# Kernel tuning notes

Hardware: AMD Instinct MI355X
Metric: run time of the kernel (lower is better)

The kernel has to match this reference:

```python
import jax, jax.numpy as jnp
import numpy as np

N = 8192          # number of candidate boxes
NUM_CLASSES = 80  # COCO-style class count
IOU_THRESHOLD = 0.45


def setup_inputs() -> dict:
    key = jax.random.key(0)
    k1, k2, k3, k4 = jax.random.split(key, 4)
    # valid xyxy boxes: top-left in [0,1000), width/height in [1,101)
    xy = jax.random.uniform(k1, (N, 2)) * 1000.0
    wh = jax.random.uniform(k2, (N, 2)) * 100.0 + 1.0
    boxes = jnp.concatenate([xy, xy + wh], axis=1)            # [N,4]
    scores = jax.random.uniform(k3, (N,))                     # [N], all > 0
    idxs = jax.random.randint(k4, (N,), 0, NUM_CLASSES)       # [N] class ids
    return {"boxes": boxes, "scores": scores, "idxs": idxs}


def _nms_keep_mask(boxes, scores, iou_thr):
    """Greedy NMS (torchvision semantics) on a single set of boxes.
    Returns a boolean keep mask in the ORIGINAL box order."""
    n = boxes.shape[0]
    order = jnp.argsort(-scores)          # score-descending priority
    b = boxes[order]                      # [n,4]
    area = (b[:, 2] - b[:, 0]) * (b[:, 3] - b[:, 1])
    lt = jnp.maximum(b[:, None, :2], b[None, :, :2])   # [n,n,2]
    rb = jnp.minimum(b[:, None, 2:], b[None, :, 2:])   # [n,n,2]
    wh = jnp.clip(rb - lt, 0.0)
    inter = wh[..., 0] * wh[..., 1]                    # [n,n]
    iou = inter / (area[:, None] + area[None, :] - inter)
    over = iou > iou_thr                               # [n,n] bool
    lower_priority = jnp.arange(n)

    def body(i, suppressed):
        kept_i = jnp.logical_not(suppressed[i])
        # a kept box suppresses all lower-priority boxes it overlaps too much
        return suppressed | (kept_i & over[i] & (lower_priority > i))

    suppressed = jax.lax.fori_loop(0, n, body, jnp.zeros((n,), bool))
    # scatter keep decisions back to original order
    return jnp.zeros((n,), bool).at[order].set(~suppressed)


def reference(boxes, scores, idxs):
    iou_threshold = IOU_THRESHOLD
    # per-class coordinate offsets make boxes of different classes disjoint,
    # so one global NMS == the per-class NMS loop of the torch module
    max_coordinate = boxes.max()
    offsets = idxs.astype(boxes.dtype) * (max_coordinate + 1.0)
    boxes_for_nms = boxes + offsets[:, None]
    keep_mask = _nms_keep_mask(boxes_for_nms, scores, iou_threshold)
    # suppressed boxes get score 0 (all real scores are > 0), so after the
    # descending sort the kept boxes occupy the leading rows exactly as in
    # the torch module; suppressed boxes pad the tail (fixed output shape).
    scores_after_nms = jnp.where(keep_mask, scores, 0.0)
    inds = jnp.argsort(-scores_after_nms)      # [N] keep indices, score-desc
    sorted_scores = scores_after_nms[inds]
    out_boxes = jnp.concatenate([boxes[inds], sorted_scores[:, None]], axis=-1)
    return (out_boxes, inds)
```

## Files before the change

kernel.cpp:

```cpp
#include <hip/hip_runtime.h>
#include <stdint.h>

#define NBOX 8192
#define NW   128
#define IOU_THR 0.45f
#define ENT_CAP 65536u
#define ENT_LDS 2560
#define TAIL_BLOCKS 8

typedef unsigned long long u64;
typedef unsigned int u32;
typedef unsigned short u16;

__global__ void __launch_bounds__(256) k_prep(const float* __restrict__ scores,
                                              const float* __restrict__ boxes,
                                              int* __restrict__ rank_part,
                                              float* __restrict__ blockmax,
                                              u32* __restrict__ cursor) {
    __shared__ u64 lk[1024];
    __shared__ float red[128];
    int t = threadIdx.x, b = blockIdx.x;
    int jc = b & 31, ip = b >> 5;
    for (int i = t; i < 1024; i += 256) {
        int gi = ip * 1024 + i;
        lk[i] = ((u64)(~__float_as_uint(scores[gi])) << 32) | (u32)gi;
    }
    if (t < 128) red[t] = boxes[b * 128 + t];
    __syncthreads();
    int j = jc * 256 + t;
    u64 kj = ((u64)(~__float_as_uint(scores[j])) << 32) | (u32)j;
    int cnt = 0;
#pragma unroll 8
    for (int i = 0; i < 1024; ++i) cnt += (lk[i] < kj) ? 1 : 0;
    rank_part[ip * NBOX + j] = cnt;
    if (t < 64) red[t] = fmaxf(red[t], red[t + 64]);
    __syncthreads();
    if (t < 64) {
        float m = red[t];
        for (int d = 32; d > 0; d >>= 1) m = fmaxf(m, __shfl_down(m, d, 64));
        if (t == 0) blockmax[b] = m;
    }
    if (b == 0 && t == 0) *cursor = 0u;
}

__global__ void __launch_bounds__(256) k_mask(const float4* __restrict__ boxes4,
                                              const int* __restrict__ idxs,
                                              const float* __restrict__ blockmax,
                                              ulonglong2* __restrict__ ent, u32* __restrict__ cursor) {
    __shared__ float4 ib[64];
    __shared__ float  ia[64];
    __shared__ int    ic[64];
    __shared__ float  red[256];
    int t = threadIdx.x;
    int w = blockIdx.x;
    int jb = blockIdx.y * 256;
    if (w * 64 >= jb + 255) return;

    red[t] = blockmax[t];
    __syncthreads();
    for (int s = 128; s > 0; s >>= 1) {
        if (t < s) red[t] = fmaxf(red[t], red[t + s]);
        __syncthreads();
    }
    float mc1 = red[0] + 1.0f;

    if (t < 64) {
        int i = w * 64 + t;
        float4 bi = boxes4[i];
        int c = idxs[i];
        float off = (float)c * mc1;
        bi.x += off; bi.y += off; bi.z += off; bi.w += off;
        ib[t] = bi;
        ia[t] = (bi.z - bi.x) * (bi.w - bi.y);
        ic[t] = c;
    }
    __syncthreads();
    int j = jb + t;
    if (w * 64 >= j) return;
    float4 bj = boxes4[j];
    int cj = idxs[j];
    float offj = (float)cj * mc1;
    bj.x += offj; bj.y += offj; bj.z += offj; bj.w += offj;
    float aj = (bj.z - bj.x) * (bj.w - bj.y);
    u64 word = 0;
    int nb = min(64, j - w * 64);
    for (int bb = 0; bb < nb; ++bb) {
        if (ic[bb] == cj) {
            float4 bi = ib[bb];
            float ltx = fmaxf(bi.x, bj.x), lty = fmaxf(bi.y, bj.y);
            float rbx = fminf(bi.z, bj.z), rby = fminf(bi.w, bj.w);
            float wx = fmaxf(rbx - ltx, 0.0f), wy = fmaxf(rby - lty, 0.0f);
            float inter = wx * wy;
            if (inter > 0.0f) {
                float iou = inter / (ia[bb] + aj - inter);
                if (iou > IOU_THR) word |= (1ULL << bb);
            }
        }
    }
    if (word) {
        u32 idx = atomicAdd(cursor, 1u);
        if (idx < ENT_CAP) {
            ulonglong2 e; e.x = word; e.y = (u64)(((u32)j << 7) | (u32)w);
            ent[idx] = e;
        }
    }
}

__global__ void __launch_bounds__(1024)
k_tail(const ulonglong2* __restrict__ ent, const u32* __restrict__ cursor,
       const int* __restrict__ rank_part, const float4* __restrict__ boxes4,
       const float* __restrict__ scores, u64* __restrict__ gLT, float* __restrict__ out) {
    __shared__ ulonglong2 sE[ENT_LDS];
    __shared__ u64 sLT[ENT_LDS];
    __shared__ u16 rank16[NBOX];
    __shared__ u64 kw[NW], sup[NW], kws[NW];
    __shared__ u32 wps[NW], wpo[NW];
    __shared__ u32 s_n, s_nk;
    __shared__ int chg;

    int t = threadIdx.x;
    if (t == 0) { u32 nn = *cursor; if (nn > ENT_CAP) nn = ENT_CAP; s_n = nn; }
    if (t < NW) { kw[t] = ~0ULL; kws[t] = 0ULL; }
    for (int j = t; j < NBOX; j += 1024) {
        int r = 0;
#pragma unroll
        for (int p = 0; p < 8; ++p) r += rank_part[p * NBOX + j];
        rank16[j] = (u16)r;
    }
    __syncthreads();
    u32 n = s_n;
    bool fits = (n <= (u32)ENT_LDS);

    for (u32 e = t; e < n; e += 1024) {
        ulonglong2 E = ent[e];
        u32 meta = (u32)E.y;
        u32 ej = meta >> 7, ew = meta & 127u;
        u32 rj = rank16[ej];
        u64 lt = 0, wrem = E.x;
        while (wrem) {
            int bb = __ffsll(wrem) - 1;
            wrem &= wrem - 1;
            if (rank16[ew * 64 + bb] < rj) lt |= (1ULL << bb);
        }
        if (fits) { sE[e] = E; sLT[e] = lt; }
        else      { gLT[e] = lt; }
    }
    __syncthreads();

    for (int iter = 0; iter < NBOX; ++iter) {
        if (t < NW) sup[t] = 0ULL;
        if (t == 0) chg = 0;
        __syncthreads();
        for (u32 e = t; e < n; e += 1024) {
            ulonglong2 E = fits ? sE[e] : ent[e];
            u64 lt      = fits ? sLT[e] : gLT[e];
            u32 meta = (u32)E.y;
            u32 ej = meta >> 7, ew = meta & 127u;
            u64 word = E.x;
            if (word & lt & kw[ew])
                atomicOr(&sup[ej >> 6], 1ULL << (ej & 63u));
            u64 rev = word & ~lt;
            if (rev && ((kw[ej >> 6] >> (ej & 63u)) & 1ULL))
                atomicOr(&sup[ew], rev);
        }
        __syncthreads();
        if (t < NW) {
            u64 nk2 = ~sup[t];
            if (nk2 != kw[t]) { kw[t] = nk2; chg = 1; }
        }
        __syncthreads();
        int dn = !chg;
        __syncthreads();
        if (dn) break;
    }

    for (int j = t; j < NBOX; j += 1024) {
        if ((kw[j >> 6] >> (j & 63)) & 1ULL) {
            u32 r = rank16[j];
            atomicOr(&kws[r >> 6], 1ULL << (r & 63u));
        }
    }
    __syncthreads();
    if (t < 64) {
        int l = t;
        u32 a0 = (u32)__popcll(kws[2 * l]), a1 = (u32)__popcll(kws[2 * l + 1]);
        u32 s = a0 + a1;
        for (int d = 1; d < 64; d <<= 1) { u32 v = __shfl_up(s, d, 64); if (l >= d) s += v; }
        u32 ex = s - a0 - a1;
        wps[2 * l] = ex; wps[2 * l + 1] = ex + a0;
        if (l == 63) s_nk = s;
        u32 b0 = (u32)__popcll(kw[2 * l]), b1 = (u32)__popcll(kw[2 * l + 1]);
        u32 so = b0 + b1;
        for (int d = 1; d < 64; d <<= 1) { u32 v = __shfl_up(so, d, 64); if (l >= d) so += v; }
        u32 exo = so - b0 - b1;
        wpo[2 * l] = exo; wpo[2 * l + 1] = exo + b0;
    }
    __syncthreads();
    u32 nk = s_nk;

    int j = blockIdx.x * 1024 + t;
    if (j < NBOX) {
        bool kept = (kw[j >> 6] >> (j & 63)) & 1ULL;
        u32 pos;
        if (kept) {
            u32 r = rank16[j];
            pos = wps[r >> 6] + (u32)__popcll(kws[r >> 6] & ((1ULL << (r & 63)) - 1ULL));
        } else {
            u32 prefO = wpo[j >> 6] + (u32)__popcll(kw[j >> 6] & ((1ULL << (j & 63)) - 1ULL));
            pos = nk + (u32)j - prefO;
        }
        float4 bx = boxes4[j];
        float s = kept ? scores[j] : 0.0f;
        out[pos * 5 + 0] = bx.x;
        out[pos * 5 + 1] = bx.y;
        out[pos * 5 + 2] = bx.z;
        out[pos * 5 + 3] = bx.w;
        out[pos * 5 + 4] = s;
        out[NBOX * 5 + pos] = (float)j;
    }
}

extern "C" void kernel_launch(void* const* d_in, const int* in_sizes, int n_in,
                              void* d_out, int out_size, void* d_ws, size_t ws_size,
                              hipStream_t stream) {
    const float* boxes  = (const float*)d_in[0];
    const float* scores = (const float*)d_in[1];
    const int*   idxs   = (const int*)d_in[2];
    float* out = (float*)d_out;

    char* w = (char*)d_ws;
    ulonglong2* ent       = (ulonglong2*)(w + 0);
    u64*        gLT       = (u64*)       (w + 1048576);
    int*        rank_part = (int*)       (w + 1572864);
    float*      blockmax  = (float*)     (w + 1835008);
    u32*        cursor    = (u32*)       (w + 1836032);

    k_prep<<<256, 256, 0, stream>>>(scores, boxes, rank_part, blockmax, cursor);
    dim3 gm(128, 32);
    k_mask<<<gm, 256, 0, stream>>>((const float4*)boxes, idxs, blockmax, ent, cursor);
    k_tail<<<TAIL_BLOCKS, 1024, 0, stream>>>(ent, cursor, rank_part, (const float4*)boxes,
                                             scores, gLT, out);
}
```

Before: 52.07 us.

## Fuse rank and mask kernels into one launch with per-segment entry buffers

```diff
diff --git a/kernel.cpp b/kernel.cpp
--- a/kernel.cpp
+++ b/kernel.cpp
@@ -4,7 +4,8 @@
 #define NBOX 8192
 #define NW   128
 #define IOU_THR 0.45f
-#define ENT_CAP 65536u
+#define SEGS 256
+#define SEGCAP 256
 #define ENT_LDS 2560
 #define TAIL_BLOCKS 8
 
@@ -12,127 +13,153 @@
 typedef unsigned int u32;
 typedef unsigned short u16;
 
-__global__ void __launch_bounds__(256) k_prep(const float* __restrict__ scores,
-                                              const float* __restrict__ boxes,
-                                              int* __restrict__ rank_part,
-                                              float* __restrict__ blockmax,
-                                              u32* __restrict__ cursor) {
-    __shared__ u64 lk[1024];
-    __shared__ float red[128];
-    int t = threadIdx.x, b = blockIdx.x;
-    int jc = b & 31, ip = b >> 5;
-    for (int i = t; i < 1024; i += 256) {
-        int gi = ip * 1024 + i;
-        lk[i] = ((u64)(~__float_as_uint(scores[gi])) << 32) | (u32)gi;
-    }
-    if (t < 128) red[t] = boxes[b * 128 + t];
-    __syncthreads();
-    int j = jc * 256 + t;
-    u64 kj = ((u64)(~__float_as_uint(scores[j])) << 32) | (u32)j;
-    int cnt = 0;
+__global__ void __launch_bounds__(256) k_pm(const float4* __restrict__ boxes4,
+                                            const int* __restrict__ idxs,
+                                            const float* __restrict__ scores,
+                                            ulonglong2* __restrict__ ent,
+                                            u32* __restrict__ entCnt,
+                                            u16* __restrict__ rank16g) {
+    int b = blockIdx.x, t = threadIdx.x;
+    if (b < SEGS) {
+        __shared__ float4 ib[64];
+        __shared__ float  ia[64];
+        __shared__ int    ic[64];
+        __shared__ float  red[256];
+        __shared__ u32    lcnt;
+        int w = b >> 1, h = b & 1;
+        float mx = 0.0f;
+        for (int i = t; i < NBOX; i += 256) {
+            float4 v = boxes4[i];
+            mx = fmaxf(mx, fmaxf(fmaxf(v.x, v.y), fmaxf(v.z, v.w)));
+        }
+        red[t] = mx;
+        __syncthreads();
+        for (int s = 128; s > 0; s >>= 1) {
+            if (t < s) red[t] = fmaxf(red[t], red[t + s]);
+            __syncthreads();
+        }
+        float mc1 = red[0] + 1.0f;
+        if (t < 64) {
+            int i = w * 64 + t;
+            float4 bi = boxes4[i];
+            int c = idxs[i];
+            float off = (float)c * mc1;
+            bi.x += off; bi.y += off; bi.z += off; bi.w += off;
+            ib[t] = bi;
+            ia[t] = (bi.z - bi.x) * (bi.w - bi.y);
+            ic[t] = c;
+        }
+        if (t == 0) lcnt = 0;
+        __syncthreads();
+        int c0   = 32 - (w >> 2);
+        int half = (c0 + 1) >> 1;
+        int beg  = (w >> 2) + (h ? half : 0);
+        int num  = h ? (c0 - half) : half;
+        for (int cc = 0; cc < num; ++cc) {
+            int j = (beg + cc) * 256 + t;
+            if (j > w * 64) {
+                float4 bj = boxes4[j];
+                int cj = idxs[j];
+                float offj = (float)cj * mc1;
+                bj.x += offj; bj.y += offj; bj.z += offj; bj.w += offj;
+                float aj = (bj.z - bj.x) * (bj.w - bj.y);
+                u64 word = 0;
+                int nb = min(64, j - w * 64);
+                for (int bb = 0; bb < nb; ++bb) {
+                    if (ic[bb] == cj) {
+                        float4 bi = ib[bb];
+                        float ltx = fmaxf(bi.x, bj.x), lty = fmaxf(bi.y, bj.y);
+                        float rbx = fminf(bi.z, bj.z), rby = fminf(bi.w, bj.w);
+                        float wx = fmaxf(rbx - ltx, 0.0f), wy = fmaxf(rby - lty, 0.0f);
+                        float inter = wx * wy;
+                        if (inter > 0.0f) {
+                            float iou = inter / (ia[bb] + aj - inter);
+                            if (iou > IOU_THR) word |= (1ULL << bb);
+                        }
+                    }
+                }
+                if (word) {
+                    u32 x = atomicAdd(&lcnt, 1u);
+                    if (x < SEGCAP) {
+                        ulonglong2 e; e.x = word; e.y = (u64)(((u32)j << 7) | (u32)w);
+                        ent[b * SEGCAP + x] = e;
+                    }
+                }
+            }
+        }
+        __syncthreads();
+        if (t == 0) entCnt[b] = min(lcnt, (u32)SEGCAP);
+    } else {
+        __shared__ u64 lk[2048];
+        __shared__ u16 part[256];
+        int rb = b - SEGS;
+        int jj = rb * 32 + (t & 31);
+        u64 kj = ((u64)(~__float_as_uint(scores[jj])) << 32) | (u32)jj;
+        int cnt = 0;
+        int p = t >> 5;
+        for (int ch = 0; ch < 4; ++ch) {
+            for (int i = t; i < 2048; i += 256) {
+                int g = ch * 2048 + i;
+                lk[i] = ((u64)(~__float_as_uint(scores[g])) << 32) | (u32)g;
+            }
+            __syncthreads();
+            int base = p * 256;
 #pragma unroll 8
-    for (int i = 0; i < 1024; ++i) cnt += (lk[i] < kj) ? 1 : 0;
-    rank_part[ip * NBOX + j] = cnt;
-    if (t < 64) red[t] = fmaxf(red[t], red[t + 64]);
-    __syncthreads();
-    if (t < 64) {
-        float m = red[t];
-        for (int d = 32; d > 0; d >>= 1) m = fmaxf(m, __shfl_down(m, d, 64));
-        if (t == 0) blockmax[b] = m;
-    }
-    if (b == 0 && t == 0) *cursor = 0u;
+            for (int i = 0; i < 256; ++i) cnt += (lk[base + i] < kj) ? 1 : 0;
+            __syncthreads();
+        }
+        part[t] = (u16)cnt;
+        __syncthreads();
+        if (t < 32) {
+            int s = 0;
+#pragma unroll
+            for (int q = 0; q < 8; ++q) s += part[q * 32 + t];
+            rank16g[rb * 32 + t] = (u16)s;
+        }
+    }
 }
 
-__global__ void __launch_bounds__(256) k_mask(const float4* __restrict__ boxes4,
-                                              const int* __restrict__ idxs,
-                                              const float* __restrict__ blockmax,
-                                              ulonglong2* __restrict__ ent, u32* __restrict__ cursor) {
-    __shared__ float4 ib[64];
-    __shared__ float  ia[64];
-    __shared__ int    ic[64];
-    __shared__ float  red[256];
-    int t = threadIdx.x;
-    int w = blockIdx.x;
-    int jb = blockIdx.y * 256;
-    if (w * 64 >= jb + 255) return;
-
-    red[t] = blockmax[t];
-    __syncthreads();
-    for (int s = 128; s > 0; s >>= 1) {
-        if (t < s) red[t] = fmaxf(red[t], red[t + s]);
-        __syncthreads();
-    }
-    float mc1 = red[0] + 1.0f;
-
-    if (t < 64) {
-        int i = w * 64 + t;
-        float4 bi = boxes4[i];
-        int c = idxs[i];
-        float off = (float)c * mc1;
-        bi.x += off; bi.y += off; bi.z += off; bi.w += off;
-        ib[t] = bi;
-        ia[t] = (bi.z - bi.x) * (bi.w - bi.y);
-        ic[t] = c;
-    }
-    __syncthreads();
-    int j = jb + t;
-    if (w * 64 >= j) return;
-    float4 bj = boxes4[j];
-    int cj = idxs[j];
-    float offj = (float)cj * mc1;
-    bj.x += offj; bj.y += offj; bj.z += offj; bj.w += offj;
-    float aj = (bj.z - bj.x) * (bj.w - bj.y);
-    u64 word = 0;
-    int nb = min(64, j - w * 64);
-    for (int bb = 0; bb < nb; ++bb) {
-        if (ic[bb] == cj) {
-            float4 bi = ib[bb];
-            float ltx = fmaxf(bi.x, bj.x), lty = fmaxf(bi.y, bj.y);
-            float rbx = fminf(bi.z, bj.z), rby = fminf(bi.w, bj.w);
-            float wx = fmaxf(rbx - ltx, 0.0f), wy = fmaxf(rby - lty, 0.0f);
-            float inter = wx * wy;
-            if (inter > 0.0f) {
-                float iou = inter / (ia[bb] + aj - inter);
-                if (iou > IOU_THR) word |= (1ULL << bb);
-            }
-        }
-    }
-    if (word) {
-        u32 idx = atomicAdd(cursor, 1u);
-        if (idx < ENT_CAP) {
-            ulonglong2 e; e.x = word; e.y = (u64)(((u32)j << 7) | (u32)w);
-            ent[idx] = e;
-        }
-    }
-}
-
 __global__ void __launch_bounds__(1024)
-k_tail(const ulonglong2* __restrict__ ent, const u32* __restrict__ cursor,
-       const int* __restrict__ rank_part, const float4* __restrict__ boxes4,
-       const float* __restrict__ scores, u64* __restrict__ gLT, float* __restrict__ out) {
+k_tail(const ulonglong2* __restrict__ ent, const u32* __restrict__ entCnt,
+       const u16* __restrict__ rank16g, const float4* __restrict__ boxes4,
+       const float* __restrict__ scores, ulonglong2* __restrict__ gEnt,
+       u64* __restrict__ gLT, float* __restrict__ out) {
     __shared__ ulonglong2 sE[ENT_LDS];
     __shared__ u64 sLT[ENT_LDS];
     __shared__ u16 rank16[NBOX];
+    __shared__ u32 scnt[SEGS], soff[SEGS];
     __shared__ u64 kw[NW], sup[NW], kws[NW];
     __shared__ u32 wps[NW], wpo[NW];
-    __shared__ u32 s_n, s_nk;
+    __shared__ u32 s_nk;
     __shared__ int chg;
 
     int t = threadIdx.x;
-    if (t == 0) { u32 nn = *cursor; if (nn > ENT_CAP) nn = ENT_CAP; s_n = nn; }
+    if (t < SEGS) scnt[t] = entCnt[t];
+    for (int j = t; j < NBOX; j += 1024) rank16[j] = rank16g[j];
     if (t < NW) { kw[t] = ~0ULL; kws[t] = 0ULL; }
-    for (int j = t; j < NBOX; j += 1024) {
-        int r = 0;
-#pragma unroll
-        for (int p = 0; p < 8; ++p) r += rank_part[p * NBOX + j];
-        rank16[j] = (u16)r;
-    }
-    __syncthreads();
-    u32 n = s_n;
+    __syncthreads();
+    if (t < 64) {
+        u32 c0 = scnt[4 * t], c1 = scnt[4 * t + 1], c2 = scnt[4 * t + 2], c3 = scnt[4 * t + 3];
+        u32 s = c0 + c1 + c2 + c3;
+        for (int d = 1; d < 64; d <<= 1) { u32 v = __shfl_up(s, d, 64); if (t >= d) s += v; }
+        u32 ex = s - (c0 + c1 + c2 + c3);
+        soff[4 * t] = ex; soff[4 * t + 1] = ex + c0;
+        soff[4 * t + 2] = ex + c0 + c1; soff[4 * t + 3] = ex + c0 + c1 + c2;
+    }
+    __syncthreads();
+    u32 n = soff[SEGS - 1] + scnt[SEGS - 1];
     bool fits = (n <= (u32)ENT_LDS);
-
+    for (u32 idx = t; idx < SEGS * SEGCAP; idx += 1024) {
+        u32 seg = idx >> 8, l = idx & 255u;
+        if (l < scnt[seg]) {
+            ulonglong2 E = ent[idx];
+            u32 d = soff[seg] + l;
+            if (fits) sE[d] = E; else gEnt[d] = E;
+        }
+    }
+    __syncthreads();
     for (u32 e = t; e < n; e += 1024) {
-        ulonglong2 E = ent[e];
+        ulonglong2 E = fits ? sE[e] : gEnt[e];
         u32 meta = (u32)E.y;
         u32 ej = meta >> 7, ew = meta & 127u;
         u32 rj = rank16[ej];
@@ -142,8 +169,7 @@
             wrem &= wrem - 1;
             if (rank16[ew * 64 + bb] < rj) lt |= (1ULL << bb);
         }
-        if (fits) { sE[e] = E; sLT[e] = lt; }
-        else      { gLT[e] = lt; }
+        if (fits) sLT[e] = lt; else gLT[e] = lt;
     }
     __syncthreads();
 
@@ -152,7 +178,7 @@
         if (t == 0) chg = 0;
         __syncthreads();
         for (u32 e = t; e < n; e += 1024) {
-            ulonglong2 E = fits ? sE[e] : ent[e];
+            ulonglong2 E = fits ? sE[e] : gEnt[e];
             u64 lt      = fits ? sLT[e] : gLT[e];
             u32 meta = (u32)E.y;
             u32 ej = meta >> 7, ew = meta & 127u;
@@ -229,15 +255,13 @@
     float* out = (float*)d_out;
 
     char* w = (char*)d_ws;
-    ulonglong2* ent       = (ulonglong2*)(w + 0);
-    u64*        gLT       = (u64*)       (w + 1048576);
-    int*        rank_part = (int*)       (w + 1572864);
-    float*      blockmax  = (float*)     (w + 1835008);
-    u32*        cursor    = (u32*)       (w + 1836032);
-
-    k_prep<<<256, 256, 0, stream>>>(scores, boxes, rank_part, blockmax, cursor);
-    dim3 gm(128, 32);
-    k_mask<<<gm, 256, 0, stream>>>((const float4*)boxes, idxs, blockmax, ent, cursor);
-    k_tail<<<TAIL_BLOCKS, 1024, 0, stream>>>(ent, cursor, rank_part, (const float4*)boxes,
-                                             scores, gLT, out);
+    ulonglong2* ent    = (ulonglong2*)(w + 0);
+    ulonglong2* gEnt   = (ulonglong2*)(w + 1048576);
+    u64*        gLT    = (u64*)       (w + 2097152);
+    u16*        rank16 = (u16*)       (w + 2621440);
+    u32*        entCnt = (u32*)       (w + 2637824);
+
+    k_pm<<<512, 256, 0, stream>>>((const float4*)boxes, idxs, scores, ent, entCnt, rank16);
+    k_tail<<<TAIL_BLOCKS, 1024, 0, stream>>>(ent, entCnt, rank16, (const float4*)boxes,
+                                             scores, gEnt, gLT, out);
 }
```

Result: slower. 151.0 us (+189.9%).
